# Kernel tuning notes

Measured on AMD Instinct MI355X. Metric: run time of the kernel, lower is better.

Reference implementation:

```python
import jax, jax.numpy as jnp
import numpy as np

B, N, K, H = 4, 4096, 32, 128
EPS = 1e-5


def setup_inputs() -> dict:
    key = jax.random.key(0)
    ks = jax.random.split(key, 12)
    atom_encode = jax.random.normal(ks[0], (B, N, H), dtype=jnp.float32)
    atom_mask = (jax.random.uniform(ks[1], (B, N)) > 0.05).astype(jnp.float32)
    dist_neighbors = jax.random.uniform(ks[2], (B, N, K), dtype=jnp.float32) * 10.0
    edge_index = jax.random.randint(ks[3], (B, N, K), 0, N, dtype=jnp.int32)
    pad = jax.random.uniform(ks[4], (B, N, K)) < 0.1
    edge_index = jnp.where(pad, -1, edge_index)
    in0 = 2 * H + 1
    W0 = jax.random.normal(ks[5], (in0, H), dtype=jnp.float32) / np.sqrt(in0)
    b0 = jnp.zeros((H,), jnp.float32)
    W1 = jax.random.normal(ks[6], (H, H), dtype=jnp.float32) / np.sqrt(H)
    b1 = jnp.zeros((H,), jnp.float32)
    W2 = jax.random.normal(ks[7], (H, H), dtype=jnp.float32) / np.sqrt(H)
    b2 = jnp.zeros((H,), jnp.float32)
    scale = jnp.ones((1, 1, H), jnp.float32)
    shift = jnp.zeros((1, 1, H), jnp.float32)
    return {"atom_encode": atom_encode, "atom_mask": atom_mask,
            "dist_neighbors": dist_neighbors, "edge_index": edge_index,
            "W0": W0, "b0": b0, "W1": W1, "b1": b1, "W2": W2, "b2": b2,
            "scale": scale, "shift": shift}


def _mpnn(atom_encode, atom_mask, dist_neighbors, edge_index,
          W0, b0, W1, b1, W2, b2, scale, shift):
    m = atom_mask[..., None]                      # (B,N,1)
    enc = atom_encode * m                         # masked node features
    idx = jnp.where(edge_index < 0, 0, edge_index)  # clamp pad index (masked later)
    # gather neighbor features per batch: (B,N,K,H)
    src = jax.vmap(lambda e, i: e[i])(enc, idx)
    self_f = jnp.broadcast_to(enc[:, :, None, :], src.shape)
    edge_feat = jnp.concatenate([src, self_f, dist_neighbors[..., None]], axis=-1)
    # message MLP (dropout is identity in eval); torch GELU = exact erf form
    h = jax.nn.gelu(edge_feat @ W0 + b0, approximate=False)
    h = jax.nn.gelu(h @ W1 + b1, approximate=False)
    h = jax.nn.gelu(h @ W2 + b2, approximate=False)
    valid = (edge_index != -1).astype(h.dtype)[..., None]  # (B,N,K,1)
    messages = h * valid
    # masked mean aggregation over neighbors
    msum = messages.sum(axis=2)                   # (B,N,H)
    vcnt = valid.sum(axis=2)                      # (B,N,1)
    vcnt = jnp.where(vcnt == 0, 1.0, vcnt)
    upd = (atom_encode + msum / vcnt) * m
    # graph normalization over valid nodes (per-batch, per-feature)
    mf = upd * m
    counts = m.sum(axis=1, keepdims=True)         # (B,1,1)
    counts = jnp.where(counts == 0, 1.0, counts)
    mean = mf.sum(axis=1, keepdims=True) / counts
    var = ((mf - mean) ** 2).sum(axis=1, keepdims=True) / counts
    std = jnp.sqrt(var + EPS)
    out = ((upd - mean) / std * scale + shift) * m
    return out


def reference(atom_encode, atom_mask, dist_neighbors, edge_index,
              W0, b0, W1, b1, W2, b2, scale, shift):
    out = _mpnn(atom_encode, atom_mask, dist_neighbors, edge_index,
                W0, b0, W1, b1, W2, b2, scale, shift)
    return (out, atom_mask, dist_neighbors, edge_index)
```

## Files before the change

### kernel.cpp

```cpp
#include <hip/hip_runtime.h>
#include <hip/hip_bf16.h>
#include <math.h>

#define BB 4
#define NN 4096
#define KK 32
#define HH 128

#define NPB 64
#define THREADS 1024
#define NPAIR 8
#define NPI (NPB / NPAIR)
#define NBLK ((BB * NN) / NPB)
#define BPB (NBLK / BB)

typedef short bf16x8 __attribute__((ext_vector_type(8)));
typedef float f32x16 __attribute__((ext_vector_type(16)));
typedef float f32x2  __attribute__((ext_vector_type(2)));
typedef unsigned int u32;

#define OFF_W1   0
#define OFF_W2   32768
#define OFF_H0   65536
#define OFF_SELF (OFF_H0 + 65536)
#define OFF_WD   (OFF_SELF + NPB*HH*2)
#define OFF_B1   (OFF_WD + HH*2)
#define OFF_B2   (OFF_B1 + HH*4)
#define LDS_TOTAL (OFF_B2 + HH*4)

#define MFMA(a,b,c) __builtin_amdgcn_mfma_f32_32x32x16_bf16(a,b,c,0,0,0)

__device__ __forceinline__ u32 pack_bf2(float lo, float hi) {
    u32 ul, uh;
    __builtin_memcpy(&ul, &lo, 4);
    __builtin_memcpy(&uh, &hi, 4);
    return __builtin_amdgcn_perm(uh + 0x8000u, ul + 0x8000u, 0x07060302u);
}
__device__ __forceinline__ short f2bfs(float v) {
    __hip_bfloat16 h = __float2bfloat16(v);
    short r; __builtin_memcpy(&r, &h, 2); return r;
}
__device__ __forceinline__ f32x2 unpk2(u32 w) {
    u32 lo = w << 16;
    u32 hi2 = w & 0xffff0000u;
    float flo, fhi;
    __builtin_memcpy(&flo, &lo, 4);
    __builtin_memcpy(&fhi, &hi2, 4);
    return (f32x2){flo, fhi};
}
__device__ __forceinline__ f32x2 gelu2(f32x2 x) {
    f32x2 x2 = x * x;
    f32x2 t = x * (x2 * 0.10294828f + 2.30220913f);
    f32x2 e;
    e.x = __builtin_amdgcn_exp2f(t.x);
    e.y = __builtin_amdgcn_exp2f(t.y);
    f32x2 ep = e + 1.0f;
    f32x2 r;
    r.x = __builtin_amdgcn_rcpf(ep.x);
    r.y = __builtin_amdgcn_rcpf(ep.y);
    return x - x * r;
}

union frag { bf16x8 v; u32 w[4]; };

#define TRANS_MT_PL(ACC, MT, FARR, LB) do {                                     \
    u32 pk8[8];                                                                 \
    _Pragma("unroll") for (int q = 0; q < 8; ++q) {                             \
        int row0 = 8 * (q >> 1) + 2 * (q & 1) + 4 * hi;                         \
        f32x2 bb = *(const f32x2*)(s_b1f + (MT) * 32 + row0);                   \
        f32x2 av = {ACC[2*q], ACC[2*q+1]};                                      \
        f32x2 hv = gelu2(av + bb);                                              \
        pk8[q] = pack_bf2(hv.x, hv.y);                                          \
    }                                                                           \
    _Pragma("unroll") for (int e = 0; e < 2; ++e) {                             \
        _Pragma("unroll") for (int rr = 0; rr < 2; ++rr) {                      \
            u32 a_ = pk8[rr + 4*e], b_ = pk8[rr + 4*e + 2];                     \
            asm("v_permlane32_swap_b32 %0, %1" : "+v"(a_), "+v"(b_));           \
            FARR[(LB) + e].w[rr] = a_; FARR[(LB) + e].w[rr + 2] = b_;           \
        }                                                                       \
    }                                                                           \
} while (0)

__global__ __launch_bounds__(256) void prep_w0_kernel(
    const float* __restrict__ W0, short* __restrict__ W0t)
{
    int e = blockIdx.x * 256 + threadIdx.x;
    if (e >= HH * 256) return;
    int feat = e >> 8;
    int k = e & 255;
    W0t[feat * 256 + k] = f2bfs(W0[(size_t)k * HH + feat]);
}

__global__ __launch_bounds__(128) void precompute_kernel(
    const float* __restrict__ enc, const float* __restrict__ mask,
    const short* __restrict__ W0t, const float* __restrict__ b0,
    __hip_bfloat16* __restrict__ Ysrc, __hip_bfloat16* __restrict__ Yself)
{
    const int tid = threadIdx.x;
    const int wave = tid >> 6;
    const int lane = tid & 63;
    const int li = lane & 31;
    const int hi = lane >> 5;
    const int rowBase = blockIdx.x * 64 + wave * 32;
    const int myrow = rowBase + li;

    const float m = mask[myrow];
    bf16x8 A[8];
    #pragma unroll
    for (int ks = 0; ks < 8; ++ks) {
        const float* p = enc + (size_t)myrow * HH + ks * 16 + hi * 8;
        float4 a = *(const float4*)p;
        float4 c = *(const float4*)(p + 4);
        frag f;
        f.w[0] = pack_bf2(a.x * m, a.y * m);
        f.w[1] = pack_bf2(a.z * m, a.w * m);
        f.w[2] = pack_bf2(c.x * m, c.y * m);
        f.w[3] = pack_bf2(c.z * m, c.w * m);
        A[ks] = f.v;
    }

    #pragma unroll
    for (int h2 = 0; h2 < 2; ++h2) {
        __hip_bfloat16* dest = h2 ? Yself : Ysrc;
        #pragma unroll 1
        for (int mt = 0; mt < 4; ++mt) {
            const float bias = h2 ? b0[mt * 32 + li] : 0.0f;
            f32x16 acc;
            #pragma unroll
            for (int r = 0; r < 16; ++r) acc[r] = 0.f;
            #pragma unroll
            for (int ks = 0; ks < 8; ++ks) {
                bf16x8 Bf = *(const bf16x8*)(W0t + (size_t)(mt * 32 + li) * 256
                                              + h2 * HH + ks * 16 + hi * 8);
                acc = MFMA(A[ks], Bf, acc);
            }
            #pragma unroll
            for (int r = 0; r < 16; ++r) {
                int rrow = (r & 3) + 8 * (r >> 2) + 4 * hi;
                dest[(size_t)(rowBase + rrow) * HH + mt * 32 + li] =
                    __float2bfloat16(acc[r] + bias);
            }
        }
    }
}

__global__ __launch_bounds__(THREADS) void mpnn_kernel(
    const float* __restrict__ enc, const float* __restrict__ mask,
    const float* __restrict__ dist, const int* __restrict__ eidx,
    const __hip_bfloat16* __restrict__ Ysrc, const __hip_bfloat16* __restrict__ Yself,
    const float* __restrict__ W0,
    const float* __restrict__ W1, const float* __restrict__ b1,
    const float* __restrict__ W2, const float* __restrict__ b2,
    float* __restrict__ upd, float* __restrict__ psum2, float* __restrict__ psumsq2)
{
    extern __shared__ char lds[];
    const int tid  = threadIdx.x;
    const int wave = tid >> 6;
    const int lane = tid & 63;
    const int li   = lane & 31;
    const int hi   = lane >> 5;
    const int p    = wave & 1;
    const int pr   = wave >> 1;
    const int nodeBase = blockIdx.x * NPB;

    #pragma unroll
    for (int tbl = 0; tbl < 2; ++tbl) {
        const float* W = tbl ? W2 : W1;
        short* dst = (short*)(lds + tbl * 32768);
        #pragma unroll
        for (int i = 0; i < (HH * HH) / THREADS; ++i) {
            int e = i * THREADS + tid;
            int feat = e & 127, k = e >> 7;
            float v = W[(size_t)k * HH + feat];
            int mt = feat >> 5, ks = k >> 4, h2 = (k >> 3) & 1, j = k & 7;
            dst[((mt * 8 + ks) * 64 + h2 * 32 + (feat & 31)) * 8 + j] = f2bfs(v);
        }
    }
    {
        uint4* sv = (uint4*)(lds + OFF_SELF);
        sv[tid] = *(const uint4*)(Yself + (size_t)nodeBase * HH + tid * 8);
    }
    short* swd = (short*)(lds + OFF_WD);
    if (tid < HH) swd[tid] = f2bfs(W0[(size_t)256 * HH + tid]);
    float* s_b1f = (float*)(lds + OFF_B1);
    if (tid < HH) s_b1f[tid] = b1[tid];
    float* s_b2f = (float*)(lds + OFF_B2);
    if (tid < HH) s_b2f[tid] = b2[tid];
    __syncthreads();

    const int b = nodeBase >> 12;
    const __hip_bfloat16* YsB = Ysrc + (size_t)b * NN * HH;
    char* h0buf = lds + OFF_H0 + (size_t)pr * 8192;

    float st_s0 = 0.f, st_q0 = 0.f, st_s1 = 0.f, st_q1 = 0.f;

    #pragma unroll 1
    for (int i = 0; i < NPI; ++i) {
        __syncthreads();

        const int node_local = pr * NPI + i;
        const int gnode = nodeBase + node_local;

        int ie = eidx[(size_t)gnode * KK + li];
        float dste = dist[(size_t)gnode * KK + li];
        float mask_n = mask[gnode];
        bool valid = ie >= 0;
        int ic = valid ? ie : 0;
        u32 vmask = (u32)__ballot(valid);
        int vc = __popc(vmask);
        float inv_vc = 1.0f / (float)(vc < 1 ? 1 : vc);

        const char* gbase = (const char*)(YsB + (size_t)ic * HH) + hi * 16;
        const short* sself = (const short*)(lds + OFF_SELF) + node_local * HH;
        const f32x2 d2 = {dste, dste};
        #pragma unroll
        for (int kk = 0; kk < 4; ++kk) {
            const int ks = p * 4 + kk;
            frag gg; gg.v = *(const bf16x8*)(gbase + ks * 32);
            frag yy; yy.v = *(const bf16x8*)(sself + ks * 16 + hi * 8);
            frag dw; dw.v = *(const bf16x8*)(swd + ks * 16 + hi * 8);
            frag h;
            #pragma unroll
            for (int q = 0; q < 4; ++q) {
                f32x2 z = unpk2(gg.w[q]) + unpk2(yy.w[q]) + d2 * unpk2(dw.w[q]);
                f32x2 hv = gelu2(z);
                h.w[q] = pack_bf2(hv.x, hv.y);
            }
            *(bf16x8*)(h0buf + (ks * 64 + lane) * 16) = h.v;
        }
        __syncthreads();

        frag F2loc[4];
        #pragma unroll
        for (int j = 0; j < 2; ++j) {
            const int mt = 2 * p + j;
            f32x16 acc;
            #pragma unroll
            for (int r = 0; r < 16; ++r) acc[r] = 0.f;
            #pragma unroll
            for (int ks = 0; ks < 8; ++ks) {
                bf16x8 a = *(const bf16x8*)(lds + OFF_W1 + ((mt * 8 + ks) * 64 + lane) * 16);
                bf16x8 h0 = *(const bf16x8*)(h0buf + (ks * 64 + lane) * 16);
                acc = MFMA(a, h0, acc);
            }
            TRANS_MT_PL(acc, mt, F2loc, 2 * j);
        }
        __syncthreads();

        #pragma unroll
        for (int s = 0; s < 4; ++s)
            *(bf16x8*)(h0buf + ((4 * p + s) * 64 + lane) * 16) = F2loc[s].v;
        __syncthreads();

        f32x2 emask[8];
        #pragma unroll
        for (int q = 0; q < 8; ++q) {
            int e0 = ((2 * q) & 3) + 8 * (q >> 1) + 4 * hi;
            emask[q].x = (float)((vmask >> e0) & 1u);
            emask[q].y = (float)((vmask >> (e0 + 1)) & 1u);
        }

        float sres[2];
        #pragma unroll
        for (int j = 0; j < 2; ++j) {
            const int nt = 2 * p + j;
            f32x16 acc;
            #pragma unroll
            for (int r = 0; r < 16; ++r) acc[r] = 0.f;
            #pragma unroll
            for (int ks = 0; ks < 8; ++ks) {
                bf16x8 f2f = *(const bf16x8*)(h0buf + (ks * 64 + lane) * 16);
                bf16x8 w2f = *(const bf16x8*)(lds + OFF_W2 + ((nt * 8 + ks) * 64 + lane) * 16);
                acc = MFMA(f2f, w2f, acc);
            }
            float bv = s_b2f[nt * 32 + li];
            const f32x2 bv2 = {bv, bv};
            f32x2 tacc = {0.f, 0.f};
            #pragma unroll
            for (int q = 0; q < 8; ++q) {
                f32x2 av = {acc[2*q], acc[2*q+1]};
                f32x2 v2 = gelu2(av + bv2);
                tacc += v2 * emask[q];
            }
            float t = tacc.x + tacc.y;
            t += __shfl_xor(t, 32, 64);
            sres[j] = t;
        }

        int f0 = (2 * p) * 32 + li;
        int f1 = (2 * p + 1) * 32 + li;
        float u0 = (enc[(size_t)gnode * HH + f0] + sres[0] * inv_vc) * mask_n;
        float u1 = (enc[(size_t)gnode * HH + f1] + sres[1] * inv_vc) * mask_n;
        upd[(size_t)gnode * HH + f0] = u0;
        upd[(size_t)gnode * HH + f1] = u1;
        if (hi == 0) {
            st_s0 += u0; st_q0 = fmaf(u0, u0, st_q0);
            st_s1 += u1; st_q1 = fmaf(u1, u1, st_q1);
        }
    }

    __syncthreads();
    float4* red = (float4*)(lds + OFF_H0);
    red[tid] = (hi == 0) ? make_float4(st_s0, st_q0, st_s1, st_q1)
                         : make_float4(0.f, 0.f, 0.f, 0.f);
    __syncthreads();
    if (tid < HH) {
        const int f = tid;
        const int fp = f >> 6;
        const int fs = (f >> 5) & 1;
        const int fl = f & 31;
        float s = 0.f, sq = 0.f;
        #pragma unroll
        for (int w8 = 0; w8 < 8; ++w8) {
            float4 v = red[(2 * w8 + fp) * 64 + fl];
            s  += fs ? v.z : v.x;
            sq += fs ? v.w : v.y;
        }
        psum2[(size_t)blockIdx.x * HH + f]   = s;
        psumsq2[(size_t)blockIdx.x * HH + f] = sq;
    }
}

__global__ __launch_bounds__(128) void finalize_stats_kernel(
    const float* __restrict__ psum2, const float* __restrict__ psumsq2,
    const float* __restrict__ mask, float* __restrict__ meanp, float* __restrict__ istdp)
{
    const int b = blockIdx.x;
    const int j = threadIdx.x;
    float s = 0.f, s2 = 0.f;
    #pragma unroll 4
    for (int c = 0; c < BPB; ++c) {
        s  += psum2[((size_t)(b * BPB + c)) * HH + j];
        s2 += psumsq2[((size_t)(b * BPB + c)) * HH + j];
    }
    float cpart = 0.f;
    #pragma unroll 4
    for (int t = 0; t < NN / HH; ++t)
        cpart += mask[(size_t)b * NN + (size_t)t * HH + j];
    __shared__ float red[HH];
    red[j] = cpart;
    __syncthreads();
    for (int off = HH / 2; off > 0; off >>= 1) {
        if (j < off) red[j] += red[j + off];
        __syncthreads();
    }
    float counts = red[0];
    if (counts == 0.f) counts = 1.f;
    float mean = s / counts;
    float var  = (s2 - 2.f * mean * s + (float)NN * mean * mean) / counts;
    meanp[b * HH + j] = mean;
    istdp[b * HH + j] = 1.0f / sqrtf(var + 1e-5f);
}

__global__ void write_out_kernel(
    const float* __restrict__ mask, const float* __restrict__ dist,
    const int* __restrict__ eidx, const float* __restrict__ meanp,
    const float* __restrict__ istdp, const float* __restrict__ scale,
    const float* __restrict__ shift, float* __restrict__ out)
{
    const size_t T0 = (size_t)BB * NN * HH;
    const size_t T1 = (size_t)BB * NN;
    const size_t T2 = (size_t)BB * NN * KK;
    const size_t stride = (size_t)gridDim.x * blockDim.x;
    const size_t t = (size_t)blockIdx.x * blockDim.x + threadIdx.x;

    for (size_t x = t; x < T0; x += stride) {
        int h = (int)(x & (HH - 1));
        size_t bn = x >> 7;
        int b = (int)(bn >> 12);
        float m = mask[bn];
        float v = (out[x] - meanp[b * HH + h]) * istdp[b * HH + h] * scale[h] + shift[h];
        out[x] = v * m;
    }
    float* out1 = out + T0;
    for (size_t x = t; x < T1; x += stride) out1[x] = mask[x];
    float* out2 = out1 + T1;
    for (size_t x = t; x < T2; x += stride) out2[x] = dist[x];
    float* out3 = out2 + T2;
    for (size_t x = t; x < T2; x += stride) out3[x] = (float)eidx[x];
}

extern "C" void kernel_launch(void* const* d_in, const int* in_sizes, int n_in,
                              void* d_out, int out_size, void* d_ws, size_t ws_size,
                              hipStream_t stream) {
    const float* enc   = (const float*)d_in[0];
    const float* mask  = (const float*)d_in[1];
    const float* dist  = (const float*)d_in[2];
    const int*   eidx  = (const int*)  d_in[3];
    const float* W0    = (const float*)d_in[4];
    const float* b0    = (const float*)d_in[5];
    const float* W1    = (const float*)d_in[6];
    const float* b1    = (const float*)d_in[7];
    const float* W2    = (const float*)d_in[8];
    const float* b2    = (const float*)d_in[9];
    const float* scale = (const float*)d_in[10];
    const float* shift = (const float*)d_in[11];
    float* out = (float*)d_out;
    float* upd = out;

    const size_t T0 = (size_t)BB * NN * HH;
    const size_t T1 = (size_t)BB * NN;

    __hip_bfloat16* Ysrc  = (__hip_bfloat16*)d_ws;
    __hip_bfloat16* Yself = (__hip_bfloat16*)(out + T0 + T1);
    float* wsf     = (float*)((char*)d_ws + (size_t)BB * NN * HH * 2);
    float* psum2   = wsf;
    float* psumsq2 = psum2 + (size_t)NBLK * HH;
    float* meanp   = psumsq2 + (size_t)NBLK * HH;
    float* istdp   = meanp + (size_t)BB * HH;
    short* W0t     = (short*)(istdp + (size_t)BB * HH);

    hipFuncSetAttribute((const void*)mpnn_kernel,
                        hipFuncAttributeMaxDynamicSharedMemorySize, LDS_TOTAL);

    prep_w0_kernel<<<dim3(128), dim3(256), 0, stream>>>(W0, W0t);
    precompute_kernel<<<dim3(256), dim3(128), 0, stream>>>(enc, mask, W0t, b0, Ysrc, Yself);
    mpnn_kernel<<<dim3(NBLK), dim3(THREADS), LDS_TOTAL, stream>>>(
        enc, mask, dist, eidx, Ysrc, Yself, W0, W1, b1, W2, b2, upd, psum2, psumsq2);
    finalize_stats_kernel<<<dim3(BB), dim3(128), 0, stream>>>(psum2, psumsq2, mask, meanp, istdp);
    write_out_kernel<<<dim3(1024), dim3(256), 0, stream>>>(
        mask, dist, eidx, meanp, istdp, scale, shift, out);
}
```

Baseline: 123.9 us.

## Prefetch next node's edge indices and gathered neighbor rows during compute

Software-pipelines the per-node loop: the edge index, distance, mask and four gathered neighbor feature vectors for the next node are loaded into registers while the current node's layer-1 and layer-2 MFMAs run, hiding the global gather latency. The layer-2 MFMA also takes its A fragments from registers (F2loc) for the k-slices this wave wrote itself, skipping those LDS reads. This raises register pressure and may lower occupancy.

```diff
diff --git a/kernel.cpp b/kernel.cpp
--- a/kernel.cpp
+++ b/kernel.cpp
@@ -194,6 +194,17 @@
 
     float st_s0 = 0.f, st_q0 = 0.f, st_s1 = 0.f, st_q1 = 0.f;
 
+    int   ie = eidx[(size_t)(nodeBase + pr * NPI) * KK + li];
+    float dd = dist[(size_t)(nodeBase + pr * NPI) * KK + li];
+    float mk = mask[nodeBase + pr * NPI];
+    bf16x8 g[4];
+    {
+        int ic0 = ie < 0 ? 0 : ie;
+        const char* gb = (const char*)(YsB + (size_t)ic0 * HH) + hi * 16 + p * 128;
+        #pragma unroll
+        for (int kk = 0; kk < 4; ++kk) g[kk] = *(const bf16x8*)(gb + kk * 32);
+    }
+
     #pragma unroll 1
     for (int i = 0; i < NPI; ++i) {
         __syncthreads();
@@ -201,22 +212,19 @@
         const int node_local = pr * NPI + i;
         const int gnode = nodeBase + node_local;
 
-        int ie = eidx[(size_t)gnode * KK + li];
-        float dste = dist[(size_t)gnode * KK + li];
-        float mask_n = mask[gnode];
         bool valid = ie >= 0;
-        int ic = valid ? ie : 0;
         u32 vmask = (u32)__ballot(valid);
         int vc = __popc(vmask);
         float inv_vc = 1.0f / (float)(vc < 1 ? 1 : vc);
-
-        const char* gbase = (const char*)(YsB + (size_t)ic * HH) + hi * 16;
+        float dste = dd;
+        float mask_n = mk;
+
         const short* sself = (const short*)(lds + OFF_SELF) + node_local * HH;
         const f32x2 d2 = {dste, dste};
         #pragma unroll
         for (int kk = 0; kk < 4; ++kk) {
             const int ks = p * 4 + kk;
-            frag gg; gg.v = *(const bf16x8*)(gbase + ks * 32);
+            frag gg; gg.v = g[kk];
             frag yy; yy.v = *(const bf16x8*)(sself + ks * 16 + hi * 8);
             frag dw; dw.v = *(const bf16x8*)(swd + ks * 16 + hi * 8);
             frag h;
@@ -228,6 +236,16 @@
             }
             *(bf16x8*)(h0buf + (ks * 64 + lane) * 16) = h.v;
         }
+
+        if (i + 1 < NPI) {
+            ie = eidx[(size_t)(gnode + 1) * KK + li];
+            dd = dist[(size_t)(gnode + 1) * KK + li];
+            mk = mask[gnode + 1];
+            int icn = ie < 0 ? 0 : ie;
+            const char* gb = (const char*)(YsB + (size_t)icn * HH) + hi * 16 + p * 128;
+            #pragma unroll
+            for (int kk = 0; kk < 4; ++kk) g[kk] = *(const bf16x8*)(gb + kk * 32);
+        }
         __syncthreads();
 
         frag F2loc[4];
@@ -269,7 +287,9 @@
             for (int r = 0; r < 16; ++r) acc[r] = 0.f;
             #pragma unroll
             for (int ks = 0; ks < 8; ++ks) {
-                bf16x8 f2f = *(const bf16x8*)(h0buf + (ks * 64 + lane) * 16);
+                bf16x8 f2f = ((ks >> 2) == p)
+                    ? F2loc[ks & 3].v
+                    : *(const bf16x8*)(h0buf + (ks * 64 + lane) * 16);
                 bf16x8 w2f = *(const bf16x8*)(lds + OFF_W2 + ((nt * 8 + ks) * 64 + lane) * 16);
                 acc = MFMA(f2f, w2f, acc);
             }
```

Measured after the change: 187.8 us. 1.52x slower.
